# Kernel optimization log

Hardware: AMD Instinct MI355X
Metric: run time of the kernel (lower is better)

Reference implementation:

```python
import jax, jax.numpy as jnp
import numpy as np

NUM_EMBEDDINGS = 1024
EMBEDDING_DIM = 64
COMMITMENT_COST = 0.25
N_TOKENS = 262144


def setup_inputs() -> dict:
    key = jax.random.key(0)
    k1, k2 = jax.random.split(key)
    z = jax.random.normal(k1, (N_TOKENS, EMBEDDING_DIM), dtype=jnp.float32)
    # torch init: uniform_(-1/num_embeddings, 1/num_embeddings)
    lim = 1.0 / NUM_EMBEDDINGS
    weight = jax.random.uniform(k2, (NUM_EMBEDDINGS, EMBEDDING_DIM),
                                dtype=jnp.float32, minval=-lim, maxval=lim)
    return {"z": z, "weight": weight}


def reference(z, weight):
    flat_z = z.reshape(-1, EMBEDDING_DIM)                      # (N, D)
    # squared L2 distances to each code: (N, K)
    distances = (jnp.sum(flat_z ** 2, axis=1, keepdims=True)
                 + jnp.sum(weight ** 2, axis=1)
                 - 2.0 * flat_z @ weight.T)
    indices = jnp.argmin(distances, axis=1)                    # (N,)
    z_q = weight[indices]                                      # (N, D)
    e_latent_loss = jnp.mean((jax.lax.stop_gradient(z_q) - flat_z) ** 2)
    q_latent_loss = jnp.mean((z_q - jax.lax.stop_gradient(flat_z)) ** 2)
    loss = q_latent_loss + COMMITMENT_COST * e_latent_loss
    # straight-through estimator
    z_q_st = flat_z + jax.lax.stop_gradient(z_q - flat_z)
    z_q_st = z_q_st.reshape(z.shape)
    return (z_q_st, loss, indices)
```

## Files before the change

kernel.cpp:

```cpp
#include <hip/hip_runtime.h>
#include <stdint.h>

#define N_TOK 262144
#define DIM 64
#define K_CODES 1024
#define OUT_LOSS_OFF (N_TOK * DIM)
#define OUT_IDX_OFF (N_TOK * DIM + 1)

#define THRA 0.666f
#define WCAP 256

typedef _Float16 half8 __attribute__((ext_vector_type(8)));
typedef float f32x4 __attribute__((ext_vector_type(4)));
typedef unsigned int uint32x4 __attribute__((ext_vector_type(4)));

#define SM_WF 0
#define SM_SW2 131072
#define SM_SZ2 135168
#define SM_WL 136192
#define SM_WC 152576
#define SM_RED 152640
#define SM_BYTES 152768

__device__ __forceinline__ float np_sumsq64_stream(const float4* p) {
#pragma clang fp contract(off)
  float r[8];
  {
    float4 a = p[0], b = p[1];
    r[0] = a.x * a.x;
    r[1] = a.y * a.y;
    r[2] = a.z * a.z;
    r[3] = a.w * a.w;
    r[4] = b.x * b.x;
    r[5] = b.y * b.y;
    r[6] = b.z * b.z;
    r[7] = b.w * b.w;
  }
#pragma unroll
  for (int i = 1; i < 8; ++i) {
    float4 a = p[2 * i], b = p[2 * i + 1];
    r[0] += a.x * a.x;
    r[1] += a.y * a.y;
    r[2] += a.z * a.z;
    r[3] += a.w * a.w;
    r[4] += b.x * b.x;
    r[5] += b.y * b.y;
    r[6] += b.z * b.z;
    r[7] += b.w * b.w;
  }
  return ((r[0] + r[1]) + (r[2] + r[3])) + ((r[4] + r[5]) + (r[6] + r[7]));
}

__device__ __forceinline__ float exact_dist(const float* __restrict__ z,
                                            long long t, int c,
                                            const float* __restrict__ w,
                                            float s_z2v, float w2) {
  const float4* zp = (const float4*)(z + (size_t)t * DIM);
  const float4* wp = (const float4*)(w + (size_t)c * DIM);
  float a = 0.f;
#pragma unroll
  for (int i = 0; i < 16; ++i) {
    float4 zv = zp[i];
    float4 pv = wp[i];
    a = __builtin_fmaf(zv.x + zv.x, pv.x, a);
    a = __builtin_fmaf(zv.y + zv.y, pv.y, a);
    a = __builtin_fmaf(zv.z + zv.z, pv.z, a);
    a = __builtin_fmaf(zv.w + zv.w, pv.w, a);
  }
  return (s_z2v + w2) - a;
}

__device__ __forceinline__ void make_afrag_hi(float4 a, float4 b, half8& hi) {
  float v[8] = {a.x, a.y, a.z, a.w, b.x, b.y, b.z, b.w};
  uint32x4 uh;
#pragma unroll
  for (int j = 0; j < 4; ++j) {
    _Float16 h0 = (_Float16)(v[2 * j] + v[2 * j]);
    _Float16 h1 = (_Float16)(v[2 * j + 1] + v[2 * j + 1]);
    uh[j] = (unsigned)__builtin_bit_cast(unsigned short, h0) |
            ((unsigned)__builtin_bit_cast(unsigned short, h1) << 16);
  }
  hi = __builtin_bit_cast(half8, uh);
}

__global__ __attribute__((amdgpu_flat_work_group_size(1024, 1024),
                          amdgpu_waves_per_eu(4, 4))) void vq_main_k(
    const float* __restrict__ z, const float* __restrict__ w,
    float* __restrict__ out, double* __restrict__ loss_acc) {
#pragma clang fp contract(off)
  __shared__ __align__(16) char smem[SM_BYTES];
  char* wf = smem + SM_WF;
  float* sw2 = (float*)(smem + SM_SW2);
  float* sz2 = (float*)(smem + SM_SZ2);
  double* red = (double*)(smem + SM_RED);

  const int tid = (int)threadIdx.x;
  const int lane = tid & 63;
  const int wid = tid >> 6;

  unsigned* wl = (unsigned*)(smem + SM_WL) + wid * WCAP;
  int* wc = (int*)(smem + SM_WC) + wid;
  if (lane == 0) *wc = 0;

  {
    const int c = tid;
    const float4* wp = (const float4*)(w + (size_t)c * DIM);
    float r[8];
#pragma unroll
    for (int ch = 0; ch < 8; ++ch) {
      float4 a = wp[2 * ch], b = wp[2 * ch + 1];
      float x[8] = {a.x, a.y, a.z, a.w, b.x, b.y, b.z, b.w};
      if (ch == 0) {
#pragma unroll
        for (int j = 0; j < 8; ++j) r[j] = x[j] * x[j];
      } else {
#pragma unroll
        for (int j = 0; j < 8; ++j) r[j] += x[j] * x[j];
      }
      uint32x4 pk;
#pragma unroll
      for (int j = 0; j < 4; ++j) {
        _Float16 h0 = (_Float16)(x[2 * j] * 1024.f);
        _Float16 h1 = (_Float16)(x[2 * j + 1] * 1024.f);
        pk[j] = (unsigned)__builtin_bit_cast(unsigned short, h0) |
                ((unsigned)__builtin_bit_cast(unsigned short, h1) << 16);
      }
      *(uint32x4*)(wf + c * 128 + ((ch ^ (c & 7)) << 4)) = pk;
    }
    sw2[c] = ((r[0] + r[1]) + (r[2] + r[3])) + ((r[4] + r[5]) + (r[6] + r[7]));
  }
  if (tid < 256) {
    long long gt = (long long)blockIdx.x * 256 + tid;
    sz2[tid] = np_sumsq64_stream((const float4*)(z + (size_t)gt * DIM));
  }
  __syncthreads();

  const int wtok = wid * 16;
  const int g = lane >> 4;
  const int c15 = lane & 15;
  const int swz = c15 & 7;
  half8 ah0, ah1;
  {
    long long gA = ((long long)blockIdx.x * 256 + wtok + c15) * DIM;
    const float* zr = z + gA + g * 8;
    make_afrag_hi(*(const float4*)(zr), *(const float4*)(zr + 4), ah0);
    make_afrag_hi(*(const float4*)(zr + 32), *(const float4*)(zr + 36), ah1);
  }
  const char* b0base = wf + c15 * 128 + ((g ^ swz) << 4);
  const char* b1base = wf + c15 * 128 + (((4 + g) ^ swz) << 4);

  float M1[4];
#pragma unroll
  for (int r = 0; r < 4; ++r) M1[r] = -3.4e38f;
#pragma unroll 4
  for (int ct = 0; ct < 64; ++ct) {
    float w2c = sw2[(ct << 4) | c15];
    half8 b0 =
        __builtin_bit_cast(half8, *(const uint32x4*)(b0base + ct * 2048));
    half8 b1 =
        __builtin_bit_cast(half8, *(const uint32x4*)(b1base + ct * 2048));
    float vm = w2c * -1024.f;
    f32x4 acch = {vm, vm, vm, vm};
    acch = __builtin_amdgcn_mfma_f32_16x16x32_f16(ah0, b0, acch, 0, 0, 0);
    acch = __builtin_amdgcn_mfma_f32_16x16x32_f16(ah1, b1, acch, 0, 0, 0);
#pragma unroll
    for (int r = 0; r < 4; ++r) M1[r] = fmaxf(M1[r], acch[r]);
  }
#pragma unroll
  for (int s = 1; s <= 8; s <<= 1) {
#pragma unroll
    for (int r = 0; r < 4; ++r)
      M1[r] = fmaxf(M1[r], __shfl_xor(M1[r], s, 64));
  }
  float thr[4];
#pragma unroll
  for (int r = 0; r < 4; ++r) thr[r] = M1[r] - THRA;

  const int tb = g * 4;
#pragma unroll 4
  for (int ct = 0; ct < 64; ++ct) {
    float w2c = sw2[(ct << 4) | c15];
    half8 b0 =
        __builtin_bit_cast(half8, *(const uint32x4*)(b0base + ct * 2048));
    half8 b1 =
        __builtin_bit_cast(half8, *(const uint32x4*)(b1base + ct * 2048));
    float vm = w2c * -1024.f;
    f32x4 acch = {vm, vm, vm, vm};
    acch = __builtin_amdgcn_mfma_f32_16x16x32_f16(ah0, b0, acch, 0, 0, 0);
    acch = __builtin_amdgcn_mfma_f32_16x16x32_f16(ah1, b1, acch, 0, 0, 0);
    const int cc = (ct << 4) | c15;
    bool h0 = acch[0] >= thr[0];
    bool h1 = acch[1] >= thr[1];
    bool h2 = acch[2] >= thr[2];
    bool h3 = acch[3] >= thr[3];
    if (h0 | h1 | h2 | h3) {
      if (h0) {
        int p = atomicAdd(wc, 1);
        if (p < WCAP) wl[p] = (unsigned)(((tb + 0) << 10) | cc);
      }
      if (h1) {
        int p = atomicAdd(wc, 1);
        if (p < WCAP) wl[p] = (unsigned)(((tb + 1) << 10) | cc);
      }
      if (h2) {
        int p = atomicAdd(wc, 1);
        if (p < WCAP) wl[p] = (unsigned)(((tb + 2) << 10) | cc);
      }
      if (h3) {
        int p = atomicAdd(wc, 1);
        if (p < WCAP) wl[p] = (unsigned)(((tb + 3) << 10) | cc);
      }
    }
  }

  asm volatile("s_waitcnt lgkmcnt(0)" ::: "memory");
  int n = *wc;

  int idxw = 0;
  if (lane < 16) {
    int cnt = 0, code = 0;
    for (int e = 0; e < n && e < WCAP; ++e) {
      unsigned u = wl[e];
      if ((int)(u >> 10) == lane) {
        cnt++;
        code = (int)(u & 1023u);
      }
    }
    if (n > WCAP) {
      long long gt = (long long)blockIdx.x * 256 + wtok + lane;
      float sz2v = sz2[wtok + lane];
      float bd = 3.4e38f;
      code = 0;
      for (int c = 0; c < K_CODES; ++c) {
        float d = exact_dist(z, gt, c, w, sz2v, sw2[c]);
        if (d < bd) {
          bd = d;
          code = c;
        }
      }
    } else if (cnt >= 2) {
      long long gt = (long long)blockIdx.x * 256 + wtok + lane;
      float sz2v = sz2[wtok + lane];
      float bd = 3.4e38f;
      int bi = K_CODES;
      for (int e = 0; e < n; ++e) {
        unsigned u = wl[e];
        if ((int)(u >> 10) == lane) {
          int c = (int)(u & 1023u);
          float d = exact_dist(z, gt, c, w, sz2v, sw2[c]);
          if (d < bd || (d == bd && c < bi)) {
            bd = d;
            bi = c;
          }
        }
      }
      code = bi;
    }
    idxw = code;
  }
  const int idx = __shfl(idxw, lane >> 2, 64);

  {
    const int tok = wtok + (lane >> 2), q = lane & 3;
    const long long gt = (long long)blockIdx.x * 256 + tok;
    const float4* zp = (const float4*)(z + (size_t)gt * DIM) + q * 4;
    const float4* wp = (const float4*)(w + (size_t)idx * DIM) + q * 4;
    float4* op = (float4*)(out + (size_t)gt * DIM) + q * 4;
    double ls = 0.0;
#pragma unroll
    for (int i = 0; i < 4; ++i) {
      float4 wv = wp[i];
      float4 zv = zp[i];
      op[i] = wv;
      double d0 = (double)wv.x - (double)zv.x;
      double d1 = (double)wv.y - (double)zv.y;
      double d2 = (double)wv.z - (double)zv.z;
      double d3 = (double)wv.w - (double)zv.w;
      ls = __builtin_fma(d0, d0, ls);
      ls = __builtin_fma(d1, d1, ls);
      ls = __builtin_fma(d2, d2, ls);
      ls = __builtin_fma(d3, d3, ls);
    }
    if (q == 0) out[OUT_IDX_OFF + gt] = (float)idx;
#pragma unroll
    for (int off = 32; off > 0; off >>= 1) ls += __shfl_down(ls, off, 64);
    if (lane == 0) red[wid] = ls;
  }
  __syncthreads();
  if (tid == 0) {
    double s = 0.0;
#pragma unroll
    for (int i = 0; i < 16; ++i) s += red[i];
    atomicAdd(loss_acc, s);
  }
}

__global__ void vq_final_k(const double* __restrict__ loss_acc,
                           float* __restrict__ out) {
  out[OUT_LOSS_OFF] =
      (float)(1.25 * (*loss_acc) * (1.0 / (double)((size_t)N_TOK * DIM)));
}

extern "C" void kernel_launch(void* const* d_in, const int* in_sizes, int n_in,
                              void* d_out, int out_size, void* d_ws,
                              size_t ws_size, hipStream_t stream) {
  const float* z = (const float*)d_in[0];
  const float* w = (const float*)d_in[1];
  float* out = (float*)d_out;
  double* loss_acc = (double*)d_ws;

  hipMemsetAsync(d_ws, 0, 8, stream);
  vq_main_k<<<N_TOK / 256, 1024, 0, stream>>>(z, w, out, loss_acc);
  vq_final_k<<<1, 1, 0, stream>>>(loss_acc, out);
}
```

Baseline: 366.9 us.

## Precompute fp16 codebook once globally and read B fragments from cache instead of LDS

Adds a small pre-kernel that converts the codebook to scaled fp16 and computes code norms once into a global buffer, instead of every block rebuilding a 128KB LDS copy. The main kernel now reads B fragments directly from global memory (relying on L1/L2 caching) and keeps only norms in LDS, shrinking LDS enough to raise the occupancy hint to 8 waves per EU. Norm bias values are stored transposed so one vector LDS load serves four code tiles. This trades the per-block codebook conversion and LDS fill for global/cache load latency inside the MFMA loops.

```diff
diff --git a/kernel.cpp b/kernel.cpp
--- a/kernel.cpp
+++ b/kernel.cpp
@@ -14,13 +14,17 @@
 typedef float f32x4 __attribute__((ext_vector_type(4)));
 typedef unsigned int uint32x4 __attribute__((ext_vector_type(4)));
 
-#define SM_WF 0
-#define SM_SW2 131072
-#define SM_SZ2 135168
-#define SM_WL 136192
-#define SM_WC 152576
-#define SM_RED 152640
-#define SM_BYTES 152768
+#define GW_WF16 0
+#define GW_W2 131072
+__device__ __align__(16) char g_wprep[131072 + 4096];
+
+#define SM_SW2 0
+#define SM_SVT 4096
+#define SM_SZ2 8448
+#define SM_WL 9472
+#define SM_WC 25856
+#define SM_RED 25920
+#define SM_BYTES 26048
 
 __device__ __forceinline__ float np_sumsq64_stream(const float4* p) {
 #pragma clang fp contract(off)
@@ -83,13 +87,43 @@
   hi = __builtin_bit_cast(half8, uh);
 }
 
+__global__ __launch_bounds__(256) void vq_pre_k(const float* __restrict__ w) {
+#pragma clang fp contract(off)
+  const int c = blockIdx.x * 256 + (int)threadIdx.x;
+  const float4* wp = (const float4*)(w + (size_t)c * DIM);
+  char* wf = g_wprep + GW_WF16 + (size_t)c * 128;
+  float r[8];
+#pragma unroll
+  for (int ch = 0; ch < 8; ++ch) {
+    float4 a = wp[2 * ch], b = wp[2 * ch + 1];
+    float x[8] = {a.x, a.y, a.z, a.w, b.x, b.y, b.z, b.w};
+    if (ch == 0) {
+#pragma unroll
+      for (int j = 0; j < 8; ++j) r[j] = x[j] * x[j];
+    } else {
+#pragma unroll
+      for (int j = 0; j < 8; ++j) r[j] += x[j] * x[j];
+    }
+    uint32x4 pk;
+#pragma unroll
+    for (int j = 0; j < 4; ++j) {
+      _Float16 h0 = (_Float16)(x[2 * j] * 1024.f);
+      _Float16 h1 = (_Float16)(x[2 * j + 1] * 1024.f);
+      pk[j] = (unsigned)__builtin_bit_cast(unsigned short, h0) |
+              ((unsigned)__builtin_bit_cast(unsigned short, h1) << 16);
+    }
+    *(uint32x4*)(wf + ch * 16) = pk;
+  }
+  ((float*)(g_wprep + GW_W2))[c] =
+      ((r[0] + r[1]) + (r[2] + r[3])) + ((r[4] + r[5]) + (r[6] + r[7]));
+}
+
 __global__ __attribute__((amdgpu_flat_work_group_size(1024, 1024),
-                          amdgpu_waves_per_eu(4, 4))) void vq_main_k(
+                          amdgpu_waves_per_eu(8, 8))) void vq_main_k(
     const float* __restrict__ z, const float* __restrict__ w,
     float* __restrict__ out, double* __restrict__ loss_acc) {
 #pragma clang fp contract(off)
   __shared__ __align__(16) char smem[SM_BYTES];
-  char* wf = smem + SM_WF;
   float* sw2 = (float*)(smem + SM_SW2);
   float* sz2 = (float*)(smem + SM_SZ2);
   double* red = (double*)(smem + SM_RED);
@@ -103,31 +137,9 @@
   if (lane == 0) *wc = 0;
 
   {
-    const int c = tid;
-    const float4* wp = (const float4*)(w + (size_t)c * DIM);
-    float r[8];
-#pragma unroll
-    for (int ch = 0; ch < 8; ++ch) {
-      float4 a = wp[2 * ch], b = wp[2 * ch + 1];
-      float x[8] = {a.x, a.y, a.z, a.w, b.x, b.y, b.z, b.w};
-      if (ch == 0) {
-#pragma unroll
-        for (int j = 0; j < 8; ++j) r[j] = x[j] * x[j];
-      } else {
-#pragma unroll
-        for (int j = 0; j < 8; ++j) r[j] += x[j] * x[j];
-      }
-      uint32x4 pk;
-#pragma unroll
-      for (int j = 0; j < 4; ++j) {
-        _Float16 h0 = (_Float16)(x[2 * j] * 1024.f);
-        _Float16 h1 = (_Float16)(x[2 * j + 1] * 1024.f);
-        pk[j] = (unsigned)__builtin_bit_cast(unsigned short, h0) |
-                ((unsigned)__builtin_bit_cast(unsigned short, h1) << 16);
-      }
-      *(uint32x4*)(wf + c * 128 + ((ch ^ (c & 7)) << 4)) = pk;
-    }
-    sw2[c] = ((r[0] + r[1]) + (r[2] + r[3])) + ((r[4] + r[5]) + (r[6] + r[7]));
+    float v = ((const float*)(g_wprep + GW_W2))[tid];
+    sw2[tid] = v;
+    ((float*)(smem + SM_SVT))[(tid & 15) * 68 + (tid >> 4)] = v * -1024.f;
   }
   if (tid < 256) {
     long long gt = (long long)blockIdx.x * 256 + tid;
@@ -138,7 +150,6 @@
   const int wtok = wid * 16;
   const int g = lane >> 4;
   const int c15 = lane & 15;
-  const int swz = c15 & 7;
   half8 ah0, ah1;
   {
     long long gA = ((long long)blockIdx.x * 256 + wtok + c15) * DIM;
@@ -146,69 +157,69 @@
     make_afrag_hi(*(const float4*)(zr), *(const float4*)(zr + 4), ah0);
     make_afrag_hi(*(const float4*)(zr + 32), *(const float4*)(zr + 36), ah1);
   }
-  const char* b0base = wf + c15 * 128 + ((g ^ swz) << 4);
-  const char* b1base = wf + c15 * 128 + (((4 + g) ^ swz) << 4);
+  const char* wfg = g_wprep + GW_WF16 + c15 * 128 + g * 16;
+  const char* svtrow = smem + SM_SVT + c15 * 272;
 
   float M1[4];
 #pragma unroll
   for (int r = 0; r < 4; ++r) M1[r] = -3.4e38f;
-#pragma unroll 4
-  for (int ct = 0; ct < 64; ++ct) {
-    float w2c = sw2[(ct << 4) | c15];
-    half8 b0 =
-        __builtin_bit_cast(half8, *(const uint32x4*)(b0base + ct * 2048));
-    half8 b1 =
-        __builtin_bit_cast(half8, *(const uint32x4*)(b1base + ct * 2048));
-    float vm = w2c * -1024.f;
-    f32x4 acch = {vm, vm, vm, vm};
-    acch = __builtin_amdgcn_mfma_f32_16x16x32_f16(ah0, b0, acch, 0, 0, 0);
-    acch = __builtin_amdgcn_mfma_f32_16x16x32_f16(ah1, b1, acch, 0, 0, 0);
-#pragma unroll
-    for (int r = 0; r < 4; ++r) M1[r] = fmaxf(M1[r], acch[r]);
+  for (int ct4 = 0; ct4 < 16; ++ct4) {
+    f32x4 vmq = *(const f32x4*)(svtrow + ct4 * 16);
+#pragma unroll
+    for (int j = 0; j < 4; ++j) {
+      const uint32x4* p = (const uint32x4*)(wfg + (ct4 * 4 + j) * 2048);
+      half8 b0 = __builtin_bit_cast(half8, p[0]);
+      half8 b1 = __builtin_bit_cast(half8, p[4]);
+      f32x4 acch = {vmq[j], vmq[j], vmq[j], vmq[j]};
+      acch = __builtin_amdgcn_mfma_f32_16x16x32_f16(ah0, b0, acch, 0, 0, 0);
+      acch = __builtin_amdgcn_mfma_f32_16x16x32_f16(ah1, b1, acch, 0, 0, 0);
+#pragma unroll
+      for (int r = 0; r < 4; ++r) M1[r] = fmaxf(M1[r], acch[r]);
+    }
   }
 #pragma unroll
   for (int s = 1; s <= 8; s <<= 1) {
 #pragma unroll
-    for (int r = 0; r < 4; ++r)
-      M1[r] = fmaxf(M1[r], __shfl_xor(M1[r], s, 64));
+    for (int r = 0; r < 4; ++r) M1[r] = fmaxf(M1[r], __shfl_xor(M1[r], s, 64));
   }
   float thr[4];
 #pragma unroll
   for (int r = 0; r < 4; ++r) thr[r] = M1[r] - THRA;
 
   const int tb = g * 4;
-#pragma unroll 4
-  for (int ct = 0; ct < 64; ++ct) {
-    float w2c = sw2[(ct << 4) | c15];
-    half8 b0 =
-        __builtin_bit_cast(half8, *(const uint32x4*)(b0base + ct * 2048));
-    half8 b1 =
-        __builtin_bit_cast(half8, *(const uint32x4*)(b1base + ct * 2048));
-    float vm = w2c * -1024.f;
-    f32x4 acch = {vm, vm, vm, vm};
-    acch = __builtin_amdgcn_mfma_f32_16x16x32_f16(ah0, b0, acch, 0, 0, 0);
-    acch = __builtin_amdgcn_mfma_f32_16x16x32_f16(ah1, b1, acch, 0, 0, 0);
-    const int cc = (ct << 4) | c15;
-    bool h0 = acch[0] >= thr[0];
-    bool h1 = acch[1] >= thr[1];
-    bool h2 = acch[2] >= thr[2];
-    bool h3 = acch[3] >= thr[3];
-    if (h0 | h1 | h2 | h3) {
-      if (h0) {
-        int p = atomicAdd(wc, 1);
-        if (p < WCAP) wl[p] = (unsigned)(((tb + 0) << 10) | cc);
-      }
-      if (h1) {
-        int p = atomicAdd(wc, 1);
-        if (p < WCAP) wl[p] = (unsigned)(((tb + 1) << 10) | cc);
-      }
-      if (h2) {
-        int p = atomicAdd(wc, 1);
-        if (p < WCAP) wl[p] = (unsigned)(((tb + 2) << 10) | cc);
-      }
-      if (h3) {
-        int p = atomicAdd(wc, 1);
-        if (p < WCAP) wl[p] = (unsigned)(((tb + 3) << 10) | cc);
+  for (int ct4 = 0; ct4 < 16; ++ct4) {
+    f32x4 vmq = *(const f32x4*)(svtrow + ct4 * 16);
+#pragma unroll
+    for (int j = 0; j < 4; ++j) {
+      const int ct = ct4 * 4 + j;
+      const uint32x4* p = (const uint32x4*)(wfg + ct * 2048);
+      half8 b0 = __builtin_bit_cast(half8, p[0]);
+      half8 b1 = __builtin_bit_cast(half8, p[4]);
+      f32x4 acch = {vmq[j], vmq[j], vmq[j], vmq[j]};
+      acch = __builtin_amdgcn_mfma_f32_16x16x32_f16(ah0, b0, acch, 0, 0, 0);
+      acch = __builtin_amdgcn_mfma_f32_16x16x32_f16(ah1, b1, acch, 0, 0, 0);
+      const int cc = (ct << 4) | c15;
+      bool h0 = acch[0] >= thr[0];
+      bool h1 = acch[1] >= thr[1];
+      bool h2 = acch[2] >= thr[2];
+      bool h3 = acch[3] >= thr[3];
+      if (h0 | h1 | h2 | h3) {
+        if (h0) {
+          int q = atomicAdd(wc, 1);
+          if (q < WCAP) wl[q] = (unsigned)(((tb + 0) << 10) | cc);
+        }
+        if (h1) {
+          int q = atomicAdd(wc, 1);
+          if (q < WCAP) wl[q] = (unsigned)(((tb + 1) << 10) | cc);
+        }
+        if (h2) {
+          int q = atomicAdd(wc, 1);
+          if (q < WCAP) wl[q] = (unsigned)(((tb + 2) << 10) | cc);
+        }
+        if (h3) {
+          int q = atomicAdd(wc, 1);
+          if (q < WCAP) wl[q] = (unsigned)(((tb + 3) << 10) | cc);
+        }
       }
     }
   }
@@ -310,6 +321,7 @@
   double* loss_acc = (double*)d_ws;
 
   hipMemsetAsync(d_ws, 0, 8, stream);
+  vq_pre_k<<<4, 256, 0, stream>>>(w);
   vq_main_k<<<N_TOK / 256, 1024, 0, stream>>>(z, w, out, loss_acc);
   vq_final_k<<<1, 1, 0, stream>>>(loss_acc, out);
 }
```

After: 711.4 us. 93.9% more time.

## Split codebook staging into two halves to cut LDS and double occupancy

Applied to the files above, without the earlier changes.

The fp16 codebook is now staged in LDS one 512-code half at a time, using a code-contiguous chunk-plane layout instead of the swizzled row layout. The per-block sz2 buffer is dropped, since those norms are now computed only in the rare exact-rescore paths. The candidate list capacity is halved. Together these roughly halve LDS use, so two 1024-thread blocks can fit per CU (waves_per_eu 8) and more latency can be hidden. The costs are extra block barriers, a looser pruning threshold for the first half (more candidates), a higher chance of overflowing the smaller list into the full 1024-code fallback scan, and a tighter register budget that may cause spills.

```diff
diff --git a/kernel.cpp b/kernel.cpp
--- a/kernel.cpp
+++ b/kernel.cpp
@@ -4,23 +4,23 @@
 #define N_TOK 262144
 #define DIM 64
 #define K_CODES 1024
+#define HALF_CODES 512
 #define OUT_LOSS_OFF (N_TOK * DIM)
 #define OUT_IDX_OFF (N_TOK * DIM + 1)
 
 #define THRA 0.666f
-#define WCAP 256
+#define WCAP 128
 
 typedef _Float16 half8 __attribute__((ext_vector_type(8)));
 typedef float f32x4 __attribute__((ext_vector_type(4)));
 typedef unsigned int uint32x4 __attribute__((ext_vector_type(4)));
 
 #define SM_WF 0
-#define SM_SW2 131072
-#define SM_SZ2 135168
-#define SM_WL 136192
-#define SM_WC 152576
-#define SM_RED 152640
-#define SM_BYTES 152768
+#define SM_SW2 65536
+#define SM_WL 69632
+#define SM_WC 77824
+#define SM_RED 77888
+#define SM_BYTES 78016
 
 __device__ __forceinline__ float np_sumsq64_stream(const float4* p) {
 #pragma clang fp contract(off)
@@ -84,14 +84,13 @@
 }
 
 __global__ __attribute__((amdgpu_flat_work_group_size(1024, 1024),
-                          amdgpu_waves_per_eu(4, 4))) void vq_main_k(
+                          amdgpu_waves_per_eu(8, 8))) void vq_main_k(
     const float* __restrict__ z, const float* __restrict__ w,
     float* __restrict__ out, double* __restrict__ loss_acc) {
 #pragma clang fp contract(off)
   __shared__ __align__(16) char smem[SM_BYTES];
   char* wf = smem + SM_WF;
   float* sw2 = (float*)(smem + SM_SW2);
-  float* sz2 = (float*)(smem + SM_SZ2);
   double* red = (double*)(smem + SM_RED);
 
   const int tid = (int)threadIdx.x;
@@ -103,42 +102,13 @@
   if (lane == 0) *wc = 0;
 
   {
-    const int c = tid;
-    const float4* wp = (const float4*)(w + (size_t)c * DIM);
-    float r[8];
-#pragma unroll
-    for (int ch = 0; ch < 8; ++ch) {
-      float4 a = wp[2 * ch], b = wp[2 * ch + 1];
-      float x[8] = {a.x, a.y, a.z, a.w, b.x, b.y, b.z, b.w};
-      if (ch == 0) {
-#pragma unroll
-        for (int j = 0; j < 8; ++j) r[j] = x[j] * x[j];
-      } else {
-#pragma unroll
-        for (int j = 0; j < 8; ++j) r[j] += x[j] * x[j];
-      }
-      uint32x4 pk;
-#pragma unroll
-      for (int j = 0; j < 4; ++j) {
-        _Float16 h0 = (_Float16)(x[2 * j] * 1024.f);
-        _Float16 h1 = (_Float16)(x[2 * j + 1] * 1024.f);
-        pk[j] = (unsigned)__builtin_bit_cast(unsigned short, h0) |
-                ((unsigned)__builtin_bit_cast(unsigned short, h1) << 16);
-      }
-      *(uint32x4*)(wf + c * 128 + ((ch ^ (c & 7)) << 4)) = pk;
-    }
-    sw2[c] = ((r[0] + r[1]) + (r[2] + r[3])) + ((r[4] + r[5]) + (r[6] + r[7]));
-  }
-  if (tid < 256) {
-    long long gt = (long long)blockIdx.x * 256 + tid;
-    sz2[tid] = np_sumsq64_stream((const float4*)(z + (size_t)gt * DIM));
-  }
-  __syncthreads();
+    const float4* wp = (const float4*)(w + (size_t)tid * DIM);
+    sw2[tid] = np_sumsq64_stream(wp);
+  }
 
   const int wtok = wid * 16;
   const int g = lane >> 4;
   const int c15 = lane & 15;
-  const int swz = c15 & 7;
   half8 ah0, ah1;
   {
     long long gA = ((long long)blockIdx.x * 256 + wtok + c15) * DIM;
@@ -146,69 +116,98 @@
     make_afrag_hi(*(const float4*)(zr), *(const float4*)(zr + 4), ah0);
     make_afrag_hi(*(const float4*)(zr + 32), *(const float4*)(zr + 36), ah1);
   }
-  const char* b0base = wf + c15 * 128 + ((g ^ swz) << 4);
-  const char* b1base = wf + c15 * 128 + (((4 + g) ^ swz) << 4);
+  const char* b0base = wf + g * 8192;
+  const char* b1base = wf + (4 + g) * 8192;
 
   float M1[4];
 #pragma unroll
   for (int r = 0; r < 4; ++r) M1[r] = -3.4e38f;
+  const int tb = g * 4;
+
+#pragma unroll 1
+  for (int h = 0; h < 2; ++h) {
+    __syncthreads();
+    {
+      const int cl = tid >> 1;
+      const int hf = tid & 1;
+      const float4* wp =
+          (const float4*)(w + (size_t)(h * HALF_CODES + cl) * DIM) + hf * 8;
+#pragma unroll
+      for (int c4 = 0; c4 < 4; ++c4) {
+        float4 a = wp[2 * c4], b = wp[2 * c4 + 1];
+        float x[8] = {a.x, a.y, a.z, a.w, b.x, b.y, b.z, b.w};
+        uint32x4 pk;
+#pragma unroll
+        for (int j = 0; j < 4; ++j) {
+          _Float16 h0 = (_Float16)(x[2 * j] * 1024.f);
+          _Float16 h1 = (_Float16)(x[2 * j + 1] * 1024.f);
+          pk[j] = (unsigned)__builtin_bit_cast(unsigned short, h0) |
+                  ((unsigned)__builtin_bit_cast(unsigned short, h1) << 16);
+        }
+        *(uint32x4*)(wf + (hf * 4 + c4) * 8192 + cl * 16) = pk;
+      }
+    }
+    __syncthreads();
+
 #pragma unroll 4
-  for (int ct = 0; ct < 64; ++ct) {
-    float w2c = sw2[(ct << 4) | c15];
-    half8 b0 =
-        __builtin_bit_cast(half8, *(const uint32x4*)(b0base + ct * 2048));
-    half8 b1 =
-        __builtin_bit_cast(half8, *(const uint32x4*)(b1base + ct * 2048));
-    float vm = w2c * -1024.f;
-    f32x4 acch = {vm, vm, vm, vm};
-    acch = __builtin_amdgcn_mfma_f32_16x16x32_f16(ah0, b0, acch, 0, 0, 0);
-    acch = __builtin_amdgcn_mfma_f32_16x16x32_f16(ah1, b1, acch, 0, 0, 0);
-#pragma unroll
-    for (int r = 0; r < 4; ++r) M1[r] = fmaxf(M1[r], acch[r]);
-  }
-#pragma unroll
-  for (int s = 1; s <= 8; s <<= 1) {
-#pragma unroll
-    for (int r = 0; r < 4; ++r)
-      M1[r] = fmaxf(M1[r], __shfl_xor(M1[r], s, 64));
-  }
-  float thr[4];
-#pragma unroll
-  for (int r = 0; r < 4; ++r) thr[r] = M1[r] - THRA;
-
-  const int tb = g * 4;
-#pragma unroll 4
-  for (int ct = 0; ct < 64; ++ct) {
-    float w2c = sw2[(ct << 4) | c15];
-    half8 b0 =
-        __builtin_bit_cast(half8, *(const uint32x4*)(b0base + ct * 2048));
-    half8 b1 =
-        __builtin_bit_cast(half8, *(const uint32x4*)(b1base + ct * 2048));
-    float vm = w2c * -1024.f;
-    f32x4 acch = {vm, vm, vm, vm};
-    acch = __builtin_amdgcn_mfma_f32_16x16x32_f16(ah0, b0, acch, 0, 0, 0);
-    acch = __builtin_amdgcn_mfma_f32_16x16x32_f16(ah1, b1, acch, 0, 0, 0);
-    const int cc = (ct << 4) | c15;
-    bool h0 = acch[0] >= thr[0];
-    bool h1 = acch[1] >= thr[1];
-    bool h2 = acch[2] >= thr[2];
-    bool h3 = acch[3] >= thr[3];
-    if (h0 | h1 | h2 | h3) {
-      if (h0) {
-        int p = atomicAdd(wc, 1);
-        if (p < WCAP) wl[p] = (unsigned)(((tb + 0) << 10) | cc);
-      }
-      if (h1) {
-        int p = atomicAdd(wc, 1);
-        if (p < WCAP) wl[p] = (unsigned)(((tb + 1) << 10) | cc);
-      }
-      if (h2) {
-        int p = atomicAdd(wc, 1);
-        if (p < WCAP) wl[p] = (unsigned)(((tb + 2) << 10) | cc);
-      }
-      if (h3) {
-        int p = atomicAdd(wc, 1);
-        if (p < WCAP) wl[p] = (unsigned)(((tb + 3) << 10) | cc);
+    for (int ct = 0; ct < 32; ++ct) {
+      const int ccl = (ct << 4) | c15;
+      float w2c = sw2[(h << 9) | ccl];
+      half8 b0 =
+          __builtin_bit_cast(half8, *(const uint32x4*)(b0base + ccl * 16));
+      half8 b1 =
+          __builtin_bit_cast(half8, *(const uint32x4*)(b1base + ccl * 16));
+      float vm = w2c * -1024.f;
+      f32x4 acch = {vm, vm, vm, vm};
+      acch = __builtin_amdgcn_mfma_f32_16x16x32_f16(ah0, b0, acch, 0, 0, 0);
+      acch = __builtin_amdgcn_mfma_f32_16x16x32_f16(ah1, b1, acch, 0, 0, 0);
+#pragma unroll
+      for (int r = 0; r < 4; ++r) M1[r] = fmaxf(M1[r], acch[r]);
+    }
+#pragma unroll
+    for (int s = 1; s <= 8; s <<= 1) {
+#pragma unroll
+      for (int r = 0; r < 4; ++r)
+        M1[r] = fmaxf(M1[r], __shfl_xor(M1[r], s, 64));
+    }
+    float thr[4];
+#pragma unroll
+    for (int r = 0; r < 4; ++r) thr[r] = M1[r] - THRA;
+
+#pragma unroll 2
+    for (int ct = 0; ct < 32; ++ct) {
+      const int ccl = (ct << 4) | c15;
+      const int cc = (h << 9) | ccl;
+      float w2c = sw2[cc];
+      half8 b0 =
+          __builtin_bit_cast(half8, *(const uint32x4*)(b0base + ccl * 16));
+      half8 b1 =
+          __builtin_bit_cast(half8, *(const uint32x4*)(b1base + ccl * 16));
+      float vm = w2c * -1024.f;
+      f32x4 acch = {vm, vm, vm, vm};
+      acch = __builtin_amdgcn_mfma_f32_16x16x32_f16(ah0, b0, acch, 0, 0, 0);
+      acch = __builtin_amdgcn_mfma_f32_16x16x32_f16(ah1, b1, acch, 0, 0, 0);
+      bool h0 = acch[0] >= thr[0];
+      bool h1 = acch[1] >= thr[1];
+      bool h2 = acch[2] >= thr[2];
+      bool h3 = acch[3] >= thr[3];
+      if (h0 | h1 | h2 | h3) {
+        if (h0) {
+          int q = atomicAdd(wc, 1);
+          if (q < WCAP) wl[q] = (unsigned)(((tb + 0) << 10) | cc);
+        }
+        if (h1) {
+          int q = atomicAdd(wc, 1);
+          if (q < WCAP) wl[q] = (unsigned)(((tb + 1) << 10) | cc);
+        }
+        if (h2) {
+          int q = atomicAdd(wc, 1);
+          if (q < WCAP) wl[q] = (unsigned)(((tb + 2) << 10) | cc);
+        }
+        if (h3) {
+          int q = atomicAdd(wc, 1);
+          if (q < WCAP) wl[q] = (unsigned)(((tb + 3) << 10) | cc);
+        }
       }
     }
   }
@@ -228,7 +227,7 @@
     }
     if (n > WCAP) {
       long long gt = (long long)blockIdx.x * 256 + wtok + lane;
-      float sz2v = sz2[wtok + lane];
+      float sz2v = np_sumsq64_stream((const float4*)(z + (size_t)gt * DIM));
       float bd = 3.4e38f;
       code = 0;
       for (int c = 0; c < K_CODES; ++c) {
@@ -240,7 +239,7 @@
       }
     } else if (cnt >= 2) {
       long long gt = (long long)blockIdx.x * 256 + wtok + lane;
-      float sz2v = sz2[wtok + lane];
+      float sz2v = np_sumsq64_stream((const float4*)(z + (size_t)gt * DIM));
       float bd = 3.4e38f;
       int bi = K_CODES;
       for (int e = 0; e < n; ++e) {
```

Measured after the change: 592.6 us. 1.62x slower.
